# Kernel tuning notes

Measured on AMD Instinct MI355X. Metric: run time of the kernel, lower is better.

## Reference

```python
import jax, jax.numpy as jnp
import numpy as np

N_NODES = 100000
N_EDGES = 1600000
N_GRAPHS = 100
DIMS = [128, 128, 118, 103, 5]  # in_feats, h, h-10, h-25, num_classes


def setup_inputs() -> dict:
    key = jax.random.key(0)
    ks = jax.random.split(key, 16)
    inp = {
        "in_feat": jax.random.normal(ks[0], (N_NODES, DIMS[0]), dtype=jnp.float32),
        "src": jax.random.randint(ks[1], (N_EDGES,), 0, N_NODES, dtype=jnp.int32),
        "dst": jax.random.randint(ks[2], (N_EDGES,), 0, N_NODES, dtype=jnp.int32),
        "graph_ids": (jnp.arange(N_NODES, dtype=jnp.int32) // (N_NODES // N_GRAPHS)),
    }
    # SAGEConv params: fc_self (no bias), fc_neigh (no bias), shared bias
    for l in range(4):
        din, dout = DIMS[l], DIMS[l + 1]
        inp[f"ws{l+1}"] = jax.random.normal(ks[3 + 3 * l], (din, dout), dtype=jnp.float32) * 0.05
        inp[f"wn{l+1}"] = jax.random.normal(ks[4 + 3 * l], (din, dout), dtype=jnp.float32) * 0.05
        inp[f"b{l+1}"] = jnp.zeros((dout,), dtype=jnp.float32)
    return inp


def reference(in_feat, src, dst, graph_ids,
              ws1, wn1, b1, ws2, wn2, b2, ws3, wn3, b3, ws4, wn4, b4):
    N = in_feat.shape[0]
    # in-degree per dst node, clamped to 1 (DGL: degs.clamp(min=1))
    deg = jnp.clip(jax.ops.segment_sum(jnp.ones((src.shape[0],), in_feat.dtype), dst,
                                       num_segments=N), 1.0, None)

    def sage(h, ws, wn, b):
        # mean-aggregate neighbor features: gather over src, scatter-add to dst
        agg = jax.ops.segment_sum(h[src], dst, num_segments=N) / deg[:, None]
        return h @ ws + agg @ wn + b

    h = jax.nn.relu(sage(in_feat, ws1, wn1, b1))
    h = jax.nn.relu(sage(h, ws2, wn2, b2))
    h = jax.nn.relu(sage(h, ws3, wn3, b3))
    h = sage(h, ws4, wn4, b4)

    # dgl.mean_nodes: per-graph mean pooling over nodes
    ones = jnp.ones((N,), h.dtype)
    cnt = jax.ops.segment_sum(ones, graph_ids, num_segments=N_GRAPHS)
    pooled = jax.ops.segment_sum(h, graph_ids, num_segments=N_GRAPHS) / cnt[:, None]
    return pooled
```

## Files before the change

kernel.cpp:

```cpp
#include <hip/hip_runtime.h>
#include <cstdint>
#include <cstddef>

typedef unsigned int uint32;
typedef unsigned short ushort16;
typedef __attribute__((ext_vector_type(8))) short short8;
typedef __attribute__((ext_vector_type(4))) float floatx4;

__device__ __forceinline__ ushort16 f2bf(float f) {
    uint32 u = __builtin_bit_cast(uint32, f);
    uint32 r = (u + 0x7fffu + ((u >> 16) & 1u)) >> 16;
    return (ushort16)r;
}
__device__ __forceinline__ float bf2f(ushort16 h) {
    uint32 u = ((uint32)h) << 16;
    return __builtin_bit_cast(float, u);
}

#define PBS 4096

__global__ __launch_bounds__(256) void bucket_hist_kernel(
    const int* __restrict__ dst, int* __restrict__ bcnt, int E, int NBUCK) {
    __shared__ int l[512];
    int t = threadIdx.x;
    for (int b = t; b < NBUCK; b += 256) l[b] = 0;
    __syncthreads();
    int e0 = blockIdx.x * PBS;
    int e1 = e0 + PBS; if (e1 > E) e1 = E;
    for (int j = e0 + t; j < e1; j += 256)
        atomicAdd(&l[dst[j] >> 8], 1);
    __syncthreads();
    for (int b = t; b < NBUCK; b += 256) {
        int c = l[b];
        if (c) atomicAdd(&bcnt[b], c);
    }
}

__global__ __launch_bounds__(256) void bucket_scan_kernel(
    const int* __restrict__ bcnt, int* __restrict__ bucketOff,
    int* __restrict__ cursorA, int NBUCK, int E) {
    __shared__ int a[512], b[512];
    int t = threadIdx.x;
    a[t] = (t < NBUCK) ? bcnt[t] : 0;
    a[t + 256] = (t + 256 < NBUCK) ? bcnt[t + 256] : 0;
    __syncthreads();
    int* cur = a; int* nxt = b;
    for (int o = 1; o < 512; o <<= 1) {
#pragma unroll
        for (int i = t; i < 512; i += 256)
            nxt[i] = cur[i] + ((i >= o) ? cur[i - o] : 0);
        __syncthreads();
        int* tmp = cur; cur = nxt; nxt = tmp;
    }
#pragma unroll
    for (int i = t; i < 512; i += 256) {
        if (i <= NBUCK) {
            int off = (i == 0) ? 0 : cur[i - 1];
            bucketOff[i] = off;
            if (i < NBUCK) cursorA[i] = off;
        }
    }
    if (t == 0) bucketOff[NBUCK] = E;
}

__global__ __launch_bounds__(256) void bucket_partition_kernel(
    const int* __restrict__ src, const int* __restrict__ dst,
    int* __restrict__ cursorA, uint32* __restrict__ ebuf, int E, int NBUCK) {
    __shared__ int lbase[512];
    int tid = threadIdx.x;
    for (int b = tid; b < NBUCK; b += 256) lbase[b] = 0;
    __syncthreads();
    int e0 = blockIdx.x * PBS;
    int e1 = e0 + PBS; if (e1 > E) e1 = E;
    for (int j = e0 + tid; j < e1; j += 256)
        atomicAdd(&lbase[dst[j] >> 8], 1);
    __syncthreads();
    for (int b = tid; b < NBUCK; b += 256) {
        int c = lbase[b];
        lbase[b] = c ? atomicAdd(&cursorA[b], c) : 0;
    }
    __syncthreads();
    for (int j = e0 + tid; j < e1; j += 256) {
        int d = dst[j];
        int p = atomicAdd(&lbase[d >> 8], 1);
        ebuf[p] = ((uint32)src[j] << 8) | (uint32)(d & 255);
    }
}

__global__ __launch_bounds__(256) void bucket_build_kernel(
    const uint32* __restrict__ ebuf, const int* __restrict__ bucketOff,
    int* __restrict__ row_ptr, float* __restrict__ degf,
    int* __restrict__ csr, int N, int E) {
    __shared__ int ldeg[256];
    __shared__ int lscan[256];
    __shared__ int lcur[256];
    int b = blockIdx.x, t = threadIdx.x;
    int n0 = b << 8;
    int s = bucketOff[b], e = bucketOff[b + 1];
    ldeg[t] = 0;
    __syncthreads();
    for (int j = s + t; j < e; j += 256)
        atomicAdd(&ldeg[ebuf[j] & 255u], 1);
    __syncthreads();
    int v = ldeg[t];
    lscan[t] = v;
    __syncthreads();
    for (int off = 1; off < 256; off <<= 1) {
        int x = (t >= off) ? lscan[t - off] : 0;
        __syncthreads();
        lscan[t] += x;
        __syncthreads();
    }
    int excl = lscan[t] - v;
    int node = n0 + t;
    if (node < N) {
        row_ptr[node] = s + excl;
        degf[node] = (float)(v > 0 ? v : 1);
    }
    lcur[t] = s + excl;
    __syncthreads();
    for (int j = s + t; j < e; j += 256) {
        uint32 en = ebuf[j];
        int p = atomicAdd(&lcur[en & 255u], 1);
        csr[p] = (int)(en >> 8);
    }
    if (b == 0 && t == 0) row_ptr[N] = E;
}

__global__ void conv_bf16_kernel(const float* __restrict__ x, ushort16* __restrict__ y, int n8) {
    int i = blockIdx.x * blockDim.x + threadIdx.x;
    if (i >= n8) return;
    const float4 a = *(const float4*)(x + (size_t)i * 8);
    const float4 b = *(const float4*)(x + (size_t)i * 8 + 4);
    uint4 o;
    o.x = (uint32)f2bf(a.x) | ((uint32)f2bf(a.y) << 16);
    o.y = (uint32)f2bf(a.z) | ((uint32)f2bf(a.w) << 16);
    o.z = (uint32)f2bf(b.x) | ((uint32)f2bf(b.y) << 16);
    o.w = (uint32)f2bf(b.z) | ((uint32)f2bf(b.w) << 16);
    *(uint4*)(y + (size_t)i * 8) = o;
}

__global__ void prep_w_all_kernel(
    const float* __restrict__ W0s, const float* __restrict__ W0n,
    const float* __restrict__ W1s, const float* __restrict__ W1n,
    const float* __restrict__ W2s, const float* __restrict__ W2n,
    ushort16* __restrict__ Whi, ushort16* __restrict__ Wlo) {
    int mat = blockIdx.x >> 6;
    int idx = (blockIdx.x & 63) * 256 + threadIdx.x;
    const float* Wt[6] = {W0s, W0n, W1s, W1n, W2s, W2n};
    const int Kt[6] = {128, 128, 128, 128, 118, 118};
    const int Mt[6] = {128, 128, 118, 118, 103, 103};
    int n = idx >> 7, k = idx & 127;
    int K = Kt[mat], M = Mt[mat];
    float w = (k < K && n < M) ? Wt[mat][(size_t)k * M + n] : 0.f;
    ushort16 h = f2bf(w);
    float lo = w - bf2f(h);
    Whi[(size_t)mat * 16384 + idx] = h;
    Wlo[(size_t)mat * 16384 + idx] = f2bf(lo);
}

template<int UNROLL>
__global__ __launch_bounds__(256) void aggregate_pre_kernel(
    const ushort16* __restrict__ h,
    const int* __restrict__ row_ptr, const int* __restrict__ csr,
    const float* __restrict__ degf, ushort16* __restrict__ aggH, int N) {
    int wid = threadIdx.x >> 6;
    int lane = threadIdx.x & 63;
    int node = blockIdx.x * 4 + wid;
    if (node >= N) return;
    int s = row_ptr[node], e = row_ptr[node + 1];
    int c = lane & 15;
    int eo = lane >> 4;
    float aLo[4] = {}, aHi[4] = {};
    int j = s + eo;
    for (; j + (UNROLL - 1) * 4 < e; j += UNROLL * 4) {
        uint4 v[UNROLL];
#pragma unroll
        for (int u = 0; u < UNROLL; ++u) {
            int src_n = csr[j + u * 4];
            v[u] = *(const uint4*)(h + ((size_t)src_n << 7) + (c << 3));
        }
#pragma unroll
        for (int u = 0; u < UNROLL; ++u) {
            uint32 w[4] = {v[u].x, v[u].y, v[u].z, v[u].w};
#pragma unroll
            for (int p = 0; p < 4; ++p) {
                aLo[p] += __builtin_bit_cast(float, w[p] << 16);
                aHi[p] += __builtin_bit_cast(float, w[p] & 0xffff0000u);
            }
        }
    }
    for (; j < e; j += 4) {
        int src_n = csr[j];
        uint4 v = *(const uint4*)(h + ((size_t)src_n << 7) + (c << 3));
        uint32 w[4] = {v.x, v.y, v.z, v.w};
#pragma unroll
        for (int p = 0; p < 4; ++p) {
            aLo[p] += __builtin_bit_cast(float, w[p] << 16);
            aHi[p] += __builtin_bit_cast(float, w[p] & 0xffff0000u);
        }
    }
#pragma unroll
    for (int m = 16; m < 64; m <<= 1) {
#pragma unroll
        for (int p = 0; p < 4; ++p) {
            aLo[p] += __shfl_xor(aLo[p], m, 64);
            aHi[p] += __shfl_xor(aHi[p], m, 64);
        }
    }
    if (lane < 16) {
        float inv = 1.f / degf[node];
        uint4 ov;
        ov.x = (uint32)f2bf(aLo[0] * inv) | ((uint32)f2bf(aHi[0] * inv) << 16);
        ov.y = (uint32)f2bf(aLo[1] * inv) | ((uint32)f2bf(aHi[1] * inv) << 16);
        ov.z = (uint32)f2bf(aLo[2] * inv) | ((uint32)f2bf(aHi[2] * inv) << 16);
        ov.w = (uint32)f2bf(aLo[3] * inv) | ((uint32)f2bf(aHi[3] * inv) << 16);
        *(uint4*)(aggH + ((size_t)node << 7) + (c << 3)) = ov;
    }
}

#define RS 40
__global__ __launch_bounds__(256) void mfma_fused_kernel(
    const ushort16* __restrict__ A, const ushort16* __restrict__ G,
    const ushort16* __restrict__ Whi, const ushort16* __restrict__ Wlo,
    const float* __restrict__ bias,
    ushort16* __restrict__ Out, int N, int M) {
    __shared__ ushort16 Bs[4][64 * RS];
    const int tid = threadIdx.x;
    const int wave = tid >> 6;
    const int lane = tid & 63;
    const int quad = lane >> 4;
    const int m16 = lane & 15;
    const ushort16* Wg[4] = {Whi, Wlo, Whi + 16384, Wlo + 16384};

    floatx4 acc[4] = {};

    const int n0 = blockIdx.y * 64;
    int rowA = blockIdx.x * 64 + wave * 16 + m16;
    if (rowA >= N) rowA = N - 1;
    const ushort16* Arow = A + (size_t)rowA * 128;
    const ushort16* Grow = G + (size_t)rowA * 128;

    const int sn = tid >> 2, sh = tid & 3;
    for (int k0 = 0; k0 < 128; k0 += 32) {
#pragma unroll
        for (int mat = 0; mat < 4; ++mat) {
            const ushort16* g = Wg[mat] + (size_t)(n0 + sn) * 128 + k0 + sh * 8;
            *(uint4*)(&Bs[mat][sn * RS + sh * 8]) = *(const uint4*)g;
        }
        short8 af = *(const short8*)(Arow + k0 + quad * 8);
        short8 gf = *(const short8*)(Grow + k0 + quad * 8);
        __syncthreads();
#pragma unroll
        for (int t = 0; t < 4; ++t) {
            int nb = t * 16 + m16;
            short8 bsh = *(const short8*)(&Bs[0][nb * RS + quad * 8]);
            short8 bsl = *(const short8*)(&Bs[1][nb * RS + quad * 8]);
            short8 bnh = *(const short8*)(&Bs[2][nb * RS + quad * 8]);
            short8 bnl = *(const short8*)(&Bs[3][nb * RS + quad * 8]);
            acc[t] = __builtin_amdgcn_mfma_f32_16x16x32_bf16(af, bsh, acc[t], 0, 0, 0);
            acc[t] = __builtin_amdgcn_mfma_f32_16x16x32_bf16(gf, bnh, acc[t], 0, 0, 0);
            acc[t] = __builtin_amdgcn_mfma_f32_16x16x32_bf16(af, bsl, acc[t], 0, 0, 0);
            acc[t] = __builtin_amdgcn_mfma_f32_16x16x32_bf16(gf, bnl, acc[t], 0, 0, 0);
        }
        __syncthreads();
    }

    int rowBase = blockIdx.x * 64 + wave * 16 + quad * 4;
#pragma unroll
    for (int t = 0; t < 4; ++t) {
        int colt = n0 + t * 16 + m16;
        bool inc = (colt < M);
        float b = inc ? bias[colt] : 0.f;
#pragma unroll
        for (int r = 0; r < 4; ++r) {
            int row = rowBase + r;
            if (row < N) {
                float v = inc ? fmaxf(acc[t][r] + b, 0.f) : 0.f;
                Out[(size_t)row * 128 + colt] = f2bf(v);
            }
        }
    }
}

__global__ __launch_bounds__(256) void gemm4_kernel(
    const ushort16* __restrict__ A, const float* __restrict__ ws,
    const float* __restrict__ wn, const float* __restrict__ b4,
    float* __restrict__ Cs, float* __restrict__ Cn, int N, int K, int M) {
    __shared__ float Wsh[520], Wnh[520];
    int tid = threadIdx.x;
    for (int i = tid; i < K * M; i += 256) { Wsh[i] = ws[i]; Wnh[i] = wn[i]; }
    __syncthreads();
    int node = blockIdx.x * 256 + tid;
    if (node >= N) return;
    const ushort16* row = A + ((size_t)node << 7);
    float s[5] = {}, n[5] = {};
    for (int c8 = 0; c8 * 8 < K; ++c8) {
        uint4 v = *(const uint4*)(row + c8 * 8);
        uint32 w[4] = {v.x, v.y, v.z, v.w};
#pragma unroll
        for (int j = 0; j < 8; ++j) {
            int k = c8 * 8 + j;
            if (k < K) {
                float a = (j & 1) ? __builtin_bit_cast(float, w[j >> 1] & 0xffff0000u)
                                  : __builtin_bit_cast(float, w[j >> 1] << 16);
#pragma unroll
                for (int m = 0; m < 5; ++m) {
                    s[m] += a * Wsh[k * 5 + m];
                    n[m] += a * Wnh[k * 5 + m];
                }
            }
        }
    }
    size_t o = (size_t)node * 8;
#pragma unroll
    for (int m = 0; m < 5; ++m) {
        Cs[o + m] = s[m] + b4[m];
        Cn[o + m] = n[m];
    }
#pragma unroll
    for (int m = 5; m < 8; ++m) { Cs[o + m] = 0.f; Cn[o + m] = 0.f; }
}

template<int CPW, int UNROLL, int SLOG>
__global__ __launch_bounds__(256) void aggregate_fp32_kernel(
    const float* __restrict__ hs, const float* __restrict__ hn,
    const int* __restrict__ row_ptr, const int* __restrict__ csr,
    const float* __restrict__ degf, float* __restrict__ out, int N) {
    constexpr int EPI = 64 / CPW;
    int wid = threadIdx.x >> 6;
    int lane = threadIdx.x & 63;
    int node = blockIdx.x * 4 + wid;
    if (node >= N) return;
    int s = row_ptr[node], e = row_ptr[node + 1];
    int c = lane & (CPW - 1);
    int eo = lane / CPW;
    float4 acc = make_float4(0.f, 0.f, 0.f, 0.f);
    int j = s + eo;
    for (; j + (UNROLL - 1) * EPI < e; j += UNROLL * EPI) {
        float4 v[UNROLL];
#pragma unroll
        for (int u = 0; u < UNROLL; ++u) {
            int src_n = csr[j + u * EPI];
            v[u] = *(const float4*)(hn + ((size_t)src_n << SLOG) + (c << 2));
        }
#pragma unroll
        for (int u = 0; u < UNROLL; ++u) {
            acc.x += v[u].x; acc.y += v[u].y; acc.z += v[u].z; acc.w += v[u].w;
        }
    }
    for (; j < e; j += EPI) {
        int src_n = csr[j];
        float4 v = *(const float4*)(hn + ((size_t)src_n << SLOG) + (c << 2));
        acc.x += v.x; acc.y += v.y; acc.z += v.z; acc.w += v.w;
    }
#pragma unroll
    for (int m = CPW; m < 64; m <<= 1) {
        acc.x += __shfl_xor(acc.x, m, 64);
        acc.y += __shfl_xor(acc.y, m, 64);
        acc.z += __shfl_xor(acc.z, m, 64);
        acc.w += __shfl_xor(acc.w, m, 64);
    }
    if (lane < CPW) {
        float d = 1.f / degf[node];
        size_t o = ((size_t)node << SLOG) + (lane << 2);
        float4 hv = *(const float4*)(hs + o);
        float4 r;
        r.x = hv.x + acc.x * d;
        r.y = hv.y + acc.y * d;
        r.z = hv.z + acc.z * d;
        r.w = hv.w + acc.w * d;
        *(float4*)(out + o) = r;
    }
}

__global__ __launch_bounds__(256) void pool_kernel(
    const float* __restrict__ h, float* __restrict__ out, int npg) {
    __shared__ float sh[4][5];
    int g = blockIdx.x;
    int t = threadIdx.x;
    float acc[5] = {0.f, 0.f, 0.f, 0.f, 0.f};
    int base = g * npg;
    for (int i = t; i < npg; i += 256) {
        const float* r = h + ((size_t)(base + i) << 3);
#pragma unroll
        for (int f = 0; f < 5; ++f) acc[f] += r[f];
    }
#pragma unroll
    for (int off = 32; off > 0; off >>= 1) {
#pragma unroll
        for (int f = 0; f < 5; ++f) acc[f] += __shfl_down(acc[f], off, 64);
    }
    int wid = t >> 6, lane = t & 63;
    if (lane == 0) {
#pragma unroll
        for (int f = 0; f < 5; ++f) sh[wid][f] = acc[f];
    }
    __syncthreads();
    if (t == 0) {
        float inv = 1.f / (float)npg;
#pragma unroll
        for (int f = 0; f < 5; ++f)
            out[g * 5 + f] = (sh[0][f] + sh[1][f] + sh[2][f] + sh[3][f]) * inv;
    }
}

extern "C" void kernel_launch(void* const* d_in, const int* in_sizes, int n_in,
                              void* d_out, int out_size, void* d_ws, size_t ws_size,
                              hipStream_t stream) {
    const float* in_feat = (const float*)d_in[0];
    const int* src = (const int*)d_in[1];
    const int* dst = (const int*)d_in[2];
    const int DIMS[5] = {128, 128, 118, 103, 5};
    const int N = in_sizes[0] / 128;
    const int E = in_sizes[1];
    const int G = out_size / 5;
    const int NBUCK = (N + 255) >> 8;

    char* base = (char*)d_ws;
    size_t off = 0;
    auto carve = [&](size_t bytes) -> void* {
        off = (off + 255) & ~(size_t)255;
        void* p = base + off;
        off += bytes;
        return p;
    };
    int* bcnt = (int*)carve((size_t)NBUCK * 4);
    int* bucketOff = (int*)carve((size_t)(NBUCK + 1) * 4);
    int* cursorA = (int*)carve((size_t)NBUCK * 4);
    int* row_ptr = (int*)carve((size_t)(N + 1) * 4);
    float* degf = (float*)carve((size_t)N * 4);
    uint32* ebuf = (uint32*)carve((size_t)E * 4);
    int* csr = (int*)carve((size_t)E * 4);
    ushort16* buf0 = (ushort16*)carve((size_t)(N + 256) * 128 * 2);
    ushort16* buf1 = (ushort16*)carve((size_t)(N + 256) * 128 * 2);
    ushort16* aggH = (ushort16*)carve((size_t)(N + 256) * 128 * 2);
    ushort16* Whi = (ushort16*)carve((size_t)6 * 16384 * 2);
    ushort16* Wlo = (ushort16*)carve((size_t)6 * 16384 * 2);
    float* Cs4 = (float*)carve((size_t)N * 8 * 4);
    float* Cn4 = (float*)carve((size_t)N * 8 * 4);
    float* out4 = (float*)carve((size_t)N * 8 * 4);
    (void)n_in; (void)ws_size;

    hipMemsetAsync(bcnt, 0, (size_t)NBUCK * 4, stream);
    bucket_hist_kernel<<<(E + PBS - 1) / PBS, 256, 0, stream>>>(dst, bcnt, E, NBUCK);
    bucket_scan_kernel<<<1, 256, 0, stream>>>(bcnt, bucketOff, cursorA, NBUCK, E);
    bucket_partition_kernel<<<(E + PBS - 1) / PBS, 256, 0, stream>>>(
        src, dst, cursorA, ebuf, E, NBUCK);
    bucket_build_kernel<<<NBUCK, 256, 0, stream>>>(
        ebuf, bucketOff, row_ptr, degf, csr, N, E);

    int n8 = N * 16;
    conv_bf16_kernel<<<(n8 + 255) / 256, 256, 0, stream>>>(in_feat, buf0, n8);
    prep_w_all_kernel<<<6 * 64, 256, 0, stream>>>(
        (const float*)d_in[4], (const float*)d_in[5],
        (const float*)d_in[7], (const float*)d_in[8],
        (const float*)d_in[10], (const float*)d_in[11],
        Whi, Wlo);

    ushort16* hb[4] = {buf0, buf1, buf0, buf1};
    dim3 ggrid((N + 63) / 64, 2);
    for (int l = 0; l < 3; ++l) {
        int M = DIMS[l + 1];
        const float* b = (const float*)d_in[6 + 3 * l];
        aggregate_pre_kernel<4><<<(N + 3) / 4, 256, 0, stream>>>(
            hb[l], row_ptr, csr, degf, aggH, N);
        mfma_fused_kernel<<<ggrid, 256, 0, stream>>>(
            hb[l], aggH, Whi + (size_t)l * 2 * 16384, Wlo + (size_t)l * 2 * 16384,
            b, hb[l + 1], N, M);
    }

    gemm4_kernel<<<(N + 255) / 256, 256, 0, stream>>>(
        hb[3], (const float*)d_in[13], (const float*)d_in[14], (const float*)d_in[15],
        Cs4, Cn4, N, DIMS[3], DIMS[4]);
    aggregate_fp32_kernel<2, 1, 3><<<(N + 3) / 4, 256, 0, stream>>>(
        Cs4, Cn4, row_ptr, csr, degf, out4, N);
    pool_kernel<<<G, 256, 0, stream>>>(out4, (float*)d_out, N / G);
}
```

Baseline: 514.5 us.

## Keep weight fragments in registers and drop LDS staging in fused MFMA GEMM

The fused SAGE GEMM now has each wave load its 16-column slice of the hi/lo self and neighbor weights straight into registers once, instead of staging weight tiles through shared memory with barriers every k-step. Each block processes 128 rows in four iterations of two 16-row tiles, so the register-held weights are reused across rows and the grid's x dimension is halved. This removes the LDS traffic and __syncthreads, at the cost of more VGPRs (64 short8 weight fragments plus the A/G fragments per iteration), which may lower occupancy.

```diff
diff --git a/kernel.cpp b/kernel.cpp
--- a/kernel.cpp
+++ b/kernel.cpp
@@ -219,65 +219,75 @@
     }
 }
 
-#define RS 40
 __global__ __launch_bounds__(256) void mfma_fused_kernel(
     const ushort16* __restrict__ A, const ushort16* __restrict__ G,
     const ushort16* __restrict__ Whi, const ushort16* __restrict__ Wlo,
     const float* __restrict__ bias,
     ushort16* __restrict__ Out, int N, int M) {
-    __shared__ ushort16 Bs[4][64 * RS];
     const int tid = threadIdx.x;
     const int wave = tid >> 6;
     const int lane = tid & 63;
     const int quad = lane >> 4;
     const int m16 = lane & 15;
-    const ushort16* Wg[4] = {Whi, Wlo, Whi + 16384, Wlo + 16384};
-
-    floatx4 acc[4] = {};
-
-    const int n0 = blockIdx.y * 64;
-    int rowA = blockIdx.x * 64 + wave * 16 + m16;
-    if (rowA >= N) rowA = N - 1;
-    const ushort16* Arow = A + (size_t)rowA * 128;
-    const ushort16* Grow = G + (size_t)rowA * 128;
-
-    const int sn = tid >> 2, sh = tid & 3;
-    for (int k0 = 0; k0 < 128; k0 += 32) {
-#pragma unroll
-        for (int mat = 0; mat < 4; ++mat) {
-            const ushort16* g = Wg[mat] + (size_t)(n0 + sn) * 128 + k0 + sh * 8;
-            *(uint4*)(&Bs[mat][sn * RS + sh * 8]) = *(const uint4*)g;
-        }
-        short8 af = *(const short8*)(Arow + k0 + quad * 8);
-        short8 gf = *(const short8*)(Grow + k0 + quad * 8);
-        __syncthreads();
-#pragma unroll
-        for (int t = 0; t < 4; ++t) {
-            int nb = t * 16 + m16;
-            short8 bsh = *(const short8*)(&Bs[0][nb * RS + quad * 8]);
-            short8 bsl = *(const short8*)(&Bs[1][nb * RS + quad * 8]);
-            short8 bnh = *(const short8*)(&Bs[2][nb * RS + quad * 8]);
-            short8 bnl = *(const short8*)(&Bs[3][nb * RS + quad * 8]);
-            acc[t] = __builtin_amdgcn_mfma_f32_16x16x32_bf16(af, bsh, acc[t], 0, 0, 0);
-            acc[t] = __builtin_amdgcn_mfma_f32_16x16x32_bf16(gf, bnh, acc[t], 0, 0, 0);
-            acc[t] = __builtin_amdgcn_mfma_f32_16x16x32_bf16(af, bsl, acc[t], 0, 0, 0);
-            acc[t] = __builtin_amdgcn_mfma_f32_16x16x32_bf16(gf, bnl, acc[t], 0, 0, 0);
-        }
-        __syncthreads();
-    }
-
-    int rowBase = blockIdx.x * 64 + wave * 16 + quad * 4;
-#pragma unroll
-    for (int t = 0; t < 4; ++t) {
-        int colt = n0 + t * 16 + m16;
-        bool inc = (colt < M);
-        float b = inc ? bias[colt] : 0.f;
+
+    const int ct = blockIdx.y * 4 + wave;
+    const int colt = ct * 16 + m16;
+
+    short8 bsh[4], bsl[4], bnh[4], bnl[4];
+    {
+        const size_t wo = (size_t)colt * 128 + quad * 8;
+#pragma unroll
+        for (int ks = 0; ks < 4; ++ks) {
+            bsh[ks] = *(const short8*)(Whi + wo + ks * 32);
+            bsl[ks] = *(const short8*)(Wlo + wo + ks * 32);
+            bnh[ks] = *(const short8*)(Whi + 16384 + wo + ks * 32);
+            bnl[ks] = *(const short8*)(Wlo + 16384 + wo + ks * 32);
+        }
+    }
+    const bool inc = (colt < M);
+    const float bv = inc ? bias[colt] : 0.f;
+
+    const int r0 = blockIdx.x * 128;
+#pragma unroll
+    for (int it = 0; it < 4; ++it) {
+        const int rbase = r0 + it * 32;
+        int ra0 = rbase + m16;       if (ra0 >= N) ra0 = N - 1;
+        int ra1 = rbase + 16 + m16;  if (ra1 >= N) ra1 = N - 1;
+        const ushort16* A0 = A + ((size_t)ra0 << 7) + quad * 8;
+        const ushort16* G0 = G + ((size_t)ra0 << 7) + quad * 8;
+        const ushort16* A1 = A + ((size_t)ra1 << 7) + quad * 8;
+        const ushort16* G1 = G + ((size_t)ra1 << 7) + quad * 8;
+        short8 a0[4], g0[4], a1[4], g1[4];
+#pragma unroll
+        for (int ks = 0; ks < 4; ++ks) {
+            a0[ks] = *(const short8*)(A0 + ks * 32);
+            g0[ks] = *(const short8*)(G0 + ks * 32);
+            a1[ks] = *(const short8*)(A1 + ks * 32);
+            g1[ks] = *(const short8*)(G1 + ks * 32);
+        }
+        floatx4 acc0 = {}, acc1 = {};
+#pragma unroll
+        for (int ks = 0; ks < 4; ++ks) {
+            acc0 = __builtin_amdgcn_mfma_f32_16x16x32_bf16(a0[ks], bsh[ks], acc0, 0, 0, 0);
+            acc1 = __builtin_amdgcn_mfma_f32_16x16x32_bf16(a1[ks], bsh[ks], acc1, 0, 0, 0);
+            acc0 = __builtin_amdgcn_mfma_f32_16x16x32_bf16(g0[ks], bnh[ks], acc0, 0, 0, 0);
+            acc1 = __builtin_amdgcn_mfma_f32_16x16x32_bf16(g1[ks], bnh[ks], acc1, 0, 0, 0);
+            acc0 = __builtin_amdgcn_mfma_f32_16x16x32_bf16(a0[ks], bsl[ks], acc0, 0, 0, 0);
+            acc1 = __builtin_amdgcn_mfma_f32_16x16x32_bf16(a1[ks], bsl[ks], acc1, 0, 0, 0);
+            acc0 = __builtin_amdgcn_mfma_f32_16x16x32_bf16(g0[ks], bnl[ks], acc0, 0, 0, 0);
+            acc1 = __builtin_amdgcn_mfma_f32_16x16x32_bf16(g1[ks], bnl[ks], acc1, 0, 0, 0);
+        }
 #pragma unroll
         for (int r = 0; r < 4; ++r) {
-            int row = rowBase + r;
-            if (row < N) {
-                float v = inc ? fmaxf(acc[t][r] + b, 0.f) : 0.f;
-                Out[(size_t)row * 128 + colt] = f2bf(v);
+            int row0 = rbase + quad * 4 + r;
+            if (row0 < N) {
+                float v = inc ? fmaxf(acc0[r] + bv, 0.f) : 0.f;
+                Out[(size_t)row0 * 128 + colt] = f2bf(v);
+            }
+            int row1 = rbase + 16 + quad * 4 + r;
+            if (row1 < N) {
+                float v = inc ? fmaxf(acc1[r] + bv, 0.f) : 0.f;
+                Out[(size_t)row1 * 128 + colt] = f2bf(v);
             }
         }
     }
@@ -459,7 +469,7 @@
         Whi, Wlo);
 
     ushort16* hb[4] = {buf0, buf1, buf0, buf1};
-    dim3 ggrid((N + 63) / 64, 2);
+    dim3 ggrid((N + 127) / 128, 2);
     for (int l = 0; l < 3; ++l) {
         int M = DIMS[l + 1];
         const float* b = (const float*)d_in[6 + 3 * l];
```

Result: slower. 605.8 us (+17.7%).

## Restructure MFMA GEMM to cover full output width per block without LDS

Applied to the files above, without the earlier changes.

The fused SAGE GEMM now has each block compute all 128 output columns for 64 rows, with each wave owning two 16-column tiles. Weight fragments are loaded straight from global memory into registers instead of being staged through shared memory, which removes both __syncthreads per k-step. Dropping the second grid dimension means A and G rows are read once rather than twice, and launch_bounds adds an occupancy hint. The cost is more registers per thread and repeated per-wave global loads of the weights, which rely on cache hits. A small scan-kernel edit also removes a redundant bucketOff write.

```diff
diff --git a/kernel.cpp b/kernel.cpp
--- a/kernel.cpp
+++ b/kernel.cpp
@@ -54,10 +54,10 @@
     }
 #pragma unroll
     for (int i = t; i < 512; i += 256) {
-        if (i <= NBUCK) {
+        if (i < NBUCK) {
             int off = (i == 0) ? 0 : cur[i - 1];
             bucketOff[i] = off;
-            if (i < NBUCK) cursorA[i] = off;
+            cursorA[i] = off;
         }
     }
     if (t == 0) bucketOff[NBUCK] = E;
@@ -219,65 +219,76 @@
     }
 }
 
-#define RS 40
-__global__ __launch_bounds__(256) void mfma_fused_kernel(
+__global__ __launch_bounds__(256, 3) void mfma_fused_kernel(
     const ushort16* __restrict__ A, const ushort16* __restrict__ G,
     const ushort16* __restrict__ Whi, const ushort16* __restrict__ Wlo,
     const float* __restrict__ bias,
     ushort16* __restrict__ Out, int N, int M) {
-    __shared__ ushort16 Bs[4][64 * RS];
     const int tid = threadIdx.x;
     const int wave = tid >> 6;
     const int lane = tid & 63;
     const int quad = lane >> 4;
     const int m16 = lane & 15;
-    const ushort16* Wg[4] = {Whi, Wlo, Whi + 16384, Wlo + 16384};
-
-    floatx4 acc[4] = {};
-
-    const int n0 = blockIdx.y * 64;
-    int rowA = blockIdx.x * 64 + wave * 16 + m16;
-    if (rowA >= N) rowA = N - 1;
-    const ushort16* Arow = A + (size_t)rowA * 128;
-    const ushort16* Grow = G + (size_t)rowA * 128;
-
-    const int sn = tid >> 2, sh = tid & 3;
-    for (int k0 = 0; k0 < 128; k0 += 32) {
-#pragma unroll
-        for (int mat = 0; mat < 4; ++mat) {
-            const ushort16* g = Wg[mat] + (size_t)(n0 + sn) * 128 + k0 + sh * 8;
-            *(uint4*)(&Bs[mat][sn * RS + sh * 8]) = *(const uint4*)g;
-        }
-        short8 af = *(const short8*)(Arow + k0 + quad * 8);
-        short8 gf = *(const short8*)(Grow + k0 + quad * 8);
-        __syncthreads();
-#pragma unroll
-        for (int t = 0; t < 4; ++t) {
-            int nb = t * 16 + m16;
-            short8 bsh = *(const short8*)(&Bs[0][nb * RS + quad * 8]);
-            short8 bsl = *(const short8*)(&Bs[1][nb * RS + quad * 8]);
-            short8 bnh = *(const short8*)(&Bs[2][nb * RS + quad * 8]);
-            short8 bnl = *(const short8*)(&Bs[3][nb * RS + quad * 8]);
-            acc[t] = __builtin_amdgcn_mfma_f32_16x16x32_bf16(af, bsh, acc[t], 0, 0, 0);
-            acc[t] = __builtin_amdgcn_mfma_f32_16x16x32_bf16(gf, bnh, acc[t], 0, 0, 0);
-            acc[t] = __builtin_amdgcn_mfma_f32_16x16x32_bf16(af, bsl, acc[t], 0, 0, 0);
-            acc[t] = __builtin_amdgcn_mfma_f32_16x16x32_bf16(gf, bnl, acc[t], 0, 0, 0);
-        }
-        __syncthreads();
-    }
-
-    int rowBase = blockIdx.x * 64 + wave * 16 + quad * 4;
-#pragma unroll
-    for (int t = 0; t < 4; ++t) {
-        int colt = n0 + t * 16 + m16;
-        bool inc = (colt < M);
-        float b = inc ? bias[colt] : 0.f;
+
+    const int ct0 = wave * 2;
+    const int col0 = ct0 * 16 + m16;
+    const int col1 = col0 + 16;
+
+    const int r0 = blockIdx.x * 64;
+    int ra[4];
+#pragma unroll
+    for (int rt = 0; rt < 4; ++rt) {
+        int r = r0 + rt * 16 + m16;
+        ra[rt] = (r < N) ? r : (N - 1);
+    }
+
+    floatx4 acc0[4] = {};
+    floatx4 acc1[4] = {};
+
+    const size_t w0 = (size_t)col0 * 128;
+    const size_t w1 = (size_t)col1 * 128;
+
+#pragma unroll 1
+    for (int ks = 0; ks < 4; ++ks) {
+        const int ko = ks * 32 + quad * 8;
+        short8 b0sh = *(const short8*)(Whi + w0 + ko);
+        short8 b0sl = *(const short8*)(Wlo + w0 + ko);
+        short8 b0nh = *(const short8*)(Whi + 16384 + w0 + ko);
+        short8 b0nl = *(const short8*)(Wlo + 16384 + w0 + ko);
+        short8 b1sh = *(const short8*)(Whi + w1 + ko);
+        short8 b1sl = *(const short8*)(Wlo + w1 + ko);
+        short8 b1nh = *(const short8*)(Whi + 16384 + w1 + ko);
+        short8 b1nl = *(const short8*)(Wlo + 16384 + w1 + ko);
+#pragma unroll
+        for (int rt = 0; rt < 4; ++rt) {
+            short8 af = *(const short8*)(A + ((size_t)ra[rt] << 7) + ko);
+            short8 gf = *(const short8*)(G + ((size_t)ra[rt] << 7) + ko);
+            acc0[rt] = __builtin_amdgcn_mfma_f32_16x16x32_bf16(af, b0sh, acc0[rt], 0, 0, 0);
+            acc1[rt] = __builtin_amdgcn_mfma_f32_16x16x32_bf16(af, b1sh, acc1[rt], 0, 0, 0);
+            acc0[rt] = __builtin_amdgcn_mfma_f32_16x16x32_bf16(gf, b0nh, acc0[rt], 0, 0, 0);
+            acc1[rt] = __builtin_amdgcn_mfma_f32_16x16x32_bf16(gf, b1nh, acc1[rt], 0, 0, 0);
+            acc0[rt] = __builtin_amdgcn_mfma_f32_16x16x32_bf16(af, b0sl, acc0[rt], 0, 0, 0);
+            acc1[rt] = __builtin_amdgcn_mfma_f32_16x16x32_bf16(af, b1sl, acc1[rt], 0, 0, 0);
+            acc0[rt] = __builtin_amdgcn_mfma_f32_16x16x32_bf16(gf, b0nl, acc0[rt], 0, 0, 0);
+            acc1[rt] = __builtin_amdgcn_mfma_f32_16x16x32_bf16(gf, b1nl, acc1[rt], 0, 0, 0);
+        }
+    }
+
+    const bool inc0 = (col0 < M);
+    const bool inc1 = (col1 < M);
+    const float bv0 = inc0 ? bias[col0] : 0.f;
+    const float bv1 = inc1 ? bias[col1] : 0.f;
+#pragma unroll
+    for (int rt = 0; rt < 4; ++rt) {
+        const int rbase = r0 + rt * 16 + quad * 4;
 #pragma unroll
         for (int r = 0; r < 4; ++r) {
-            int row = rowBase + r;
+            int row = rbase + r;
             if (row < N) {
-                float v = inc ? fmaxf(acc[t][r] + b, 0.f) : 0.f;
-                Out[(size_t)row * 128 + colt] = f2bf(v);
+                float v0 = inc0 ? fmaxf(acc0[rt][r] + bv0, 0.f) : 0.f;
+                Out[(size_t)row * 128 + col0] = f2bf(v0);
+                float v1 = inc1 ? fmaxf(acc1[rt][r] + bv1, 0.f) : 0.f;
+                Out[(size_t)row * 128 + col1] = f2bf(v1);
             }
         }
     }
@@ -459,13 +470,12 @@
         Whi, Wlo);
 
     ushort16* hb[4] = {buf0, buf1, buf0, buf1};
-    dim3 ggrid((N + 63) / 64, 2);
     for (int l = 0; l < 3; ++l) {
         int M = DIMS[l + 1];
         const float* b = (const float*)d_in[6 + 3 * l];
         aggregate_pre_kernel<4><<<(N + 3) / 4, 256, 0, stream>>>(
             hb[l], row_ptr, csr, degf, aggH, N);
-        mfma_fused_kernel<<<ggrid, 256, 0, stream>>>(
+        mfma_fused_kernel<<<(N + 63) / 64, 256, 0, stream>>>(
             hb[l], aggH, Whi + (size_t)l * 2 * 16384, Wlo + (size_t)l * 2 * 16384,
             b, hb[l + 1], N, M);
     }
```

Result: slower. 579.4 us (+12.6%).
